# Performance work log

Hardware: AMD Instinct MI355X
Metric: run time of the kernel (lower is better)

## Reference

```python
import jax, jax.numpy as jnp
import numpy as np

DECAY = 0.25

@jax.custom_vjp
def quant4(x):
    # round(clamp(x, 0, 4)) with straight-through gradient masked to [0, 4]
    return jnp.round(jnp.clip(x, 0.0, 4.0))

def _quant4_fwd(x):
    return quant4(x), x

def _quant4_bwd(x, g):
    # grad passes where 0 <= x <= 4 (zeroed strictly outside, matching torch code)
    return (jnp.where((x < 0.0) | (x > 4.0), 0.0, g),)

quant4.defvjp(_quant4_fwd, _quant4_bwd)


def setup_inputs() -> dict:
    key = jax.random.key(0)
    x = jax.random.normal(key, (8, 16, 64, 56, 56), dtype=jnp.float32)
    return {"x": x}


def reference(x):
    # Sequential LIF scan over time (dim 0).
    # With mem_old = spike = 0, step 0 reduces to mem = x[0], matching the
    # original `if i >= 1` branch.
    def step(carry, x_t):
        mem_old, spike_prev = carry
        mem = (mem_old - jax.lax.stop_gradient(spike_prev)) * DECAY + x_t
        spike = quant4(mem)
        return (mem, spike), spike

    zeros = jnp.zeros_like(x[0])
    (_, _), output = jax.lax.scan(step, (zeros, zeros), x)
    return output
```

## Files before the change

### kernel.cpp

```cpp
#include <hip/hip_runtime.h>


constexpr int   LIF_T     = 8;
constexpr float LIF_DECAY = 0.25f;

__global__ __launch_bounds__(256) void
lif_kernel(const float4* __restrict__ x, float4* __restrict__ out, int n4)
{
    #pragma clang fp contract(off)

    const int idx    = blockIdx.x * blockDim.x + threadIdx.x;
    const int stride = gridDim.x * blockDim.x;

    for (int i = idx; i < n4; i += stride) {
        float mx = 0.f, my = 0.f, mz = 0.f, mw = 0.f;
        float sx = 0.f, sy = 0.f, sz = 0.f, sw = 0.f;

        #pragma unroll
        for (int t = 0; t < LIF_T; ++t) {
            const float4 xv = x[t * n4 + i];

            mx = (mx - sx) * LIF_DECAY + xv.x;
            my = (my - sy) * LIF_DECAY + xv.y;
            mz = (mz - sz) * LIF_DECAY + xv.z;
            mw = (mw - sw) * LIF_DECAY + xv.w;

            sx = rintf(fminf(fmaxf(mx, 0.f), 4.f));
            sy = rintf(fminf(fmaxf(my, 0.f), 4.f));
            sz = rintf(fminf(fmaxf(mz, 0.f), 4.f));
            sw = rintf(fminf(fmaxf(mw, 0.f), 4.f));

            out[t * n4 + i] = make_float4(sx, sy, sz, sw);
        }
    }
}

__global__ void
lif_kernel_tail(const float* __restrict__ x, float* __restrict__ out,
                int n_per_t, int start)
{
    #pragma clang fp contract(off)
    const int i = start + blockIdx.x * blockDim.x + threadIdx.x;
    if (i >= n_per_t) return;

    float mem = 0.f, spike = 0.f;
    #pragma unroll
    for (int t = 0; t < LIF_T; ++t) {
        mem   = (mem - spike) * LIF_DECAY + x[t * n_per_t + i];
        spike = rintf(fminf(fmaxf(mem, 0.f), 4.f));
        out[t * n_per_t + i] = spike;
    }
}

extern "C" void kernel_launch(void* const* d_in, const int* in_sizes, int n_in,
                              void* d_out, int out_size, void* d_ws, size_t ws_size,
                              hipStream_t stream)
{
    const float* x   = (const float*)d_in[0];
    float*       out = (float*)d_out;

    const int n_total = in_sizes[0];
    const int n_per_t = n_total / LIF_T;
    const int n4      = n_per_t / 4;

    if (n4 > 0) {
        const int block = 256;
        const int grid  = (n4 + block - 1) / block;
        lif_kernel<<<grid, block, 0, stream>>>(
            (const float4*)x, (float4*)out, n4);
    }

    const int tail_start = n4 * 4;
    const int tail_n     = n_per_t - tail_start;
    if (tail_n > 0) {
        const int block = 64;
        const int grid  = (tail_n + block - 1) / block;
        lif_kernel_tail<<<grid, block, 0, stream>>>(x, out, n_per_t, tail_start);
    }
}
```

Before: 180.5 us.

## Process two float4 lanes per thread, use nontemporal stores, cap grid

Each thread now handles two float4 columns (i and i+half) per iteration, doubling the loads in flight. Output stores use nontemporal hints to avoid polluting cache, and the grid is capped at 2048 blocks with a grid-stride loop. This aims to improve memory-level parallelism for a purely bandwidth-bound streaming kernel, at the cost of higher register use and fewer resident blocks.

```diff
diff --git a/kernel.cpp b/kernel.cpp
--- a/kernel.cpp
+++ b/kernel.cpp
@@ -1,36 +1,60 @@
 #include <hip/hip_runtime.h>
 
+
+#pragma clang fp contract(off)
 
 constexpr int   LIF_T     = 8;
 constexpr float LIF_DECAY = 0.25f;
 
+typedef float f32x4 __attribute__((ext_vector_type(4)));
+
+__device__ __forceinline__ float lif_q4(float m)
+{
+    #pragma clang fp contract(off)
+    return rintf(fminf(fmaxf(m, 0.f), 4.f));
+}
+
 __global__ __launch_bounds__(256) void
-lif_kernel(const float4* __restrict__ x, float4* __restrict__ out, int n4)
+lif_kernel(const f32x4* __restrict__ x, f32x4* __restrict__ out,
+           int n4, int half)
 {
     #pragma clang fp contract(off)
 
-    const int idx    = blockIdx.x * blockDim.x + threadIdx.x;
+    const int tid    = blockIdx.x * blockDim.x + threadIdx.x;
     const int stride = gridDim.x * blockDim.x;
 
-    for (int i = idx; i < n4; i += stride) {
-        float mx = 0.f, my = 0.f, mz = 0.f, mw = 0.f;
-        float sx = 0.f, sy = 0.f, sz = 0.f, sw = 0.f;
+    for (int i = tid; i < half; i += stride) {
+        const int j = i + half;
+
+        float amx = 0.f, amy = 0.f, amz = 0.f, amw = 0.f;
+        float asx = 0.f, asy = 0.f, asz = 0.f, asw = 0.f;
+        float bmx = 0.f, bmy = 0.f, bmz = 0.f, bmw = 0.f;
+        float bsx = 0.f, bsy = 0.f, bsz = 0.f, bsw = 0.f;
 
         #pragma unroll
         for (int t = 0; t < LIF_T; ++t) {
-            const float4 xv = x[t * n4 + i];
+            const f32x4 av = x[t * n4 + i];
+            const f32x4 bv = x[t * n4 + j];
 
-            mx = (mx - sx) * LIF_DECAY + xv.x;
-            my = (my - sy) * LIF_DECAY + xv.y;
-            mz = (mz - sz) * LIF_DECAY + xv.z;
-            mw = (mw - sw) * LIF_DECAY + xv.w;
+            amx = (amx - asx) * LIF_DECAY + av.x;
+            amy = (amy - asy) * LIF_DECAY + av.y;
+            amz = (amz - asz) * LIF_DECAY + av.z;
+            amw = (amw - asw) * LIF_DECAY + av.w;
 
-            sx = rintf(fminf(fmaxf(mx, 0.f), 4.f));
-            sy = rintf(fminf(fmaxf(my, 0.f), 4.f));
-            sz = rintf(fminf(fmaxf(mz, 0.f), 4.f));
-            sw = rintf(fminf(fmaxf(mw, 0.f), 4.f));
+            bmx = (bmx - bsx) * LIF_DECAY + bv.x;
+            bmy = (bmy - bsy) * LIF_DECAY + bv.y;
+            bmz = (bmz - bsz) * LIF_DECAY + bv.z;
+            bmw = (bmw - bsw) * LIF_DECAY + bv.w;
 
-            out[t * n4 + i] = make_float4(sx, sy, sz, sw);
+            asx = lif_q4(amx); asy = lif_q4(amy);
+            asz = lif_q4(amz); asw = lif_q4(amw);
+            bsx = lif_q4(bmx); bsy = lif_q4(bmy);
+            bsz = lif_q4(bmz); bsw = lif_q4(bmw);
+
+            f32x4 ao; ao.x = asx; ao.y = asy; ao.z = asz; ao.w = asw;
+            f32x4 bo; bo.x = bsx; bo.y = bsy; bo.z = bsz; bo.w = bsw;
+            __builtin_nontemporal_store(ao, &out[t * n4 + i]);
+            __builtin_nontemporal_store(bo, &out[t * n4 + j]);
         }
     }
 }
@@ -62,15 +86,17 @@
     const int n_total = in_sizes[0];
     const int n_per_t = n_total / LIF_T;
     const int n4      = n_per_t / 4;
+    const int half    = n4 / 2;
 
-    if (n4 > 0) {
+    if (half > 0) {
         const int block = 256;
-        const int grid  = (n4 + block - 1) / block;
+        int grid = (half + block - 1) / block;
+        if (grid > 2048) grid = 2048;
         lif_kernel<<<grid, block, 0, stream>>>(
-            (const float4*)x, (float4*)out, n4);
+            (const f32x4*)x, (f32x4*)out, n4, half);
     }
 
-    const int tail_start = n4 * 4;
+    const int tail_start = 2 * half * 4;
     const int tail_n     = n_per_t - tail_start;
     if (tail_n > 0) {
         const int block = 64;
```

New measurement: 180.7 us. No clear change (+0.1%).
